# Performance work log

Measured on AMD Instinct MI355X. Metric: run time of the kernel, lower is better.

Reference implementation:

```python
import jax, jax.numpy as jnp
import numpy as np

NUM_USERS = 1_000_000
NUM_ITEMS = 1_000_000
N_FACTORS = 64
RANK = 16
BATCH = 16384


def setup_inputs() -> dict:
    key = jax.random.key(0)
    ks = jax.random.split(key, 8)
    return {
        "users": jax.random.randint(ks[0], (BATCH,), 0, NUM_USERS),
        "items": jax.random.randint(ks[1], (BATCH,), 0, NUM_ITEMS),
        "user_emb": jax.random.normal(ks[2], (NUM_USERS, N_FACTORS), jnp.float32),
        "item_emb": jax.random.normal(ks[3], (NUM_ITEMS, N_FACTORS), jnp.float32),
        "user_bias": jax.random.normal(ks[4], (NUM_USERS,), jnp.float32),
        "item_bias": jax.random.normal(ks[5], (NUM_ITEMS,), jnp.float32),
        "A": jax.random.normal(ks[6], (NUM_ITEMS, RANK), jnp.float32),
        "B": jax.random.normal(ks[7], (RANK, N_FACTORS), jnp.float32) * (1.0 / np.sqrt(RANK)),
    }


def reference(users, items, user_emb, item_emb, user_bias, item_bias, A, B):
    # train=True path: full low-rank correction over ALL items, then gather
    users_e = user_emb[users]                      # [B, F]
    item_emb_mat = A @ B + item_emb                # [num_items, F]
    items_e = item_emb_mat[items]                  # [B, F]
    predictions = jnp.sum(users_e * items_e, axis=1)  # [B]
    predictions = predictions + user_bias[users] + item_bias[items]
    return predictions
```

## Files before the change

kernel.cpp:

```cpp
#include <hip/hip_runtime.h>

#define NF 64
#define RANK 16

__global__ __launch_bounds__(256) void MF_27436251087258_kernel(
    const int* __restrict__ users,
    const int* __restrict__ items,
    const float* __restrict__ user_emb,
    const float* __restrict__ item_emb,
    const float* __restrict__ user_bias,
    const float* __restrict__ item_bias,
    const float* __restrict__ A,
    const float* __restrict__ Bm,
    float* __restrict__ out,
    int batch)
{
    const int tid   = threadIdx.x;
    const int group = tid >> 4;
    const int lane  = tid & 15;
    const int i = blockIdx.x * 16 + group;
    if (i >= batch) return;

    const int u  = users[i];
    const int it = items[i];

    const float ub = user_bias[u];
    const float ib = item_bias[it];

    const float4 ue = *(const float4*)(user_emb + (size_t)u  * NF + lane * 4);
    const float4 ie = *(const float4*)(item_emb + (size_t)it * NF + lane * 4);

    const float* Arow = A + (size_t)it * RANK;
    const float4 a0 = *(const float4*)(Arow + 0);
    const float4 a1 = *(const float4*)(Arow + 4);
    const float4 a2 = *(const float4*)(Arow + 8);
    const float4 a3 = *(const float4*)(Arow + 12);
    const float ar[RANK] = { a0.x, a0.y, a0.z, a0.w,
                             a1.x, a1.y, a1.z, a1.w,
                             a2.x, a2.y, a2.z, a2.w,
                             a3.x, a3.y, a3.z, a3.w };

    float c0 = 0.f, c1 = 0.f, c2 = 0.f, c3 = 0.f;
    #pragma unroll
    for (int r = 0; r < RANK; ++r) {
        const float4 br = *(const float4*)(Bm + r * NF + lane * 4);
        c0 = fmaf(ar[r], br.x, c0);
        c1 = fmaf(ar[r], br.y, c1);
        c2 = fmaf(ar[r], br.z, c2);
        c3 = fmaf(ar[r], br.w, c3);
    }

    float p = ue.x * (ie.x + c0)
            + ue.y * (ie.y + c1)
            + ue.z * (ie.z + c2)
            + ue.w * (ie.w + c3);

    p += __shfl_xor(p, 8, 16);
    p += __shfl_xor(p, 4, 16);
    p += __shfl_xor(p, 2, 16);
    p += __shfl_xor(p, 1, 16);

    if (lane == 0) {
        out[i] = p + ub + ib;
    }
}

extern "C" void kernel_launch(void* const* d_in, const int* in_sizes, int n_in,
                              void* d_out, int out_size, void* d_ws, size_t ws_size,
                              hipStream_t stream) {
    const int*   users     = (const int*)  d_in[0];
    const int*   items     = (const int*)  d_in[1];
    const float* user_emb  = (const float*)d_in[2];
    const float* item_emb  = (const float*)d_in[3];
    const float* user_bias = (const float*)d_in[4];
    const float* item_bias = (const float*)d_in[5];
    const float* A         = (const float*)d_in[6];
    const float* Bm        = (const float*)d_in[7];
    float* out = (float*)d_out;

    const int batch = in_sizes[0];
    const int groups_per_block = 16;
    const int grid = (batch + groups_per_block - 1) / groups_per_block;

    MF_27436251087258_kernel<<<grid, 256, 0, stream>>>(
        users, items, user_emb, item_emb, user_bias, item_bias, A, Bm, out, batch);
}
```

Before: 10.82 us.

## Map one wavefront per prediction with scalar index loads

Switches the work mapping from 16 lanes per prediction with float4 loads to one 64-lane wavefront per prediction with scalar float loads. The user and item indices go through readfirstlane, so the bias and A-row loads can become scalar (SMEM) loads. A row elements are now wave-uniform while B is read per lane. The goal is to cut vector register use and let scalar loads serve the per-row data. The cost is a 4x larger grid (4 outputs per block instead of 16), narrower memory transactions, and a longer 6-step cross-wave shuffle reduction.

```diff
diff --git a/kernel.cpp b/kernel.cpp
--- a/kernel.cpp
+++ b/kernel.cpp
@@ -15,50 +15,38 @@
     float* __restrict__ out,
     int batch)
 {
-    const int tid   = threadIdx.x;
-    const int group = tid >> 4;
-    const int lane  = tid & 15;
-    const int i = blockIdx.x * 16 + group;
+    const int wave = threadIdx.x >> 6;
+    const int lane = threadIdx.x & 63;
+    const int i = blockIdx.x * 4 + wave;
     if (i >= batch) return;
 
-    const int u  = users[i];
-    const int it = items[i];
+    const int u  = __builtin_amdgcn_readfirstlane(users[i]);
+    const int it = __builtin_amdgcn_readfirstlane(items[i]);
 
     const float ub = user_bias[u];
     const float ib = item_bias[it];
+    const float* __restrict__ Arow = A + (size_t)it * RANK;
 
-    const float4 ue = *(const float4*)(user_emb + (size_t)u  * NF + lane * 4);
-    const float4 ie = *(const float4*)(item_emb + (size_t)it * NF + lane * 4);
-
-    const float* Arow = A + (size_t)it * RANK;
-    const float4 a0 = *(const float4*)(Arow + 0);
-    const float4 a1 = *(const float4*)(Arow + 4);
-    const float4 a2 = *(const float4*)(Arow + 8);
-    const float4 a3 = *(const float4*)(Arow + 12);
-    const float ar[RANK] = { a0.x, a0.y, a0.z, a0.w,
-                             a1.x, a1.y, a1.z, a1.w,
-                             a2.x, a2.y, a2.z, a2.w,
-                             a3.x, a3.y, a3.z, a3.w };
+    const float ue = user_emb[(size_t)u  * NF + lane];
+    const float ie = item_emb[(size_t)it * NF + lane];
 
     float c0 = 0.f, c1 = 0.f, c2 = 0.f, c3 = 0.f;
     #pragma unroll
-    for (int r = 0; r < RANK; ++r) {
-        const float4 br = *(const float4*)(Bm + r * NF + lane * 4);
-        c0 = fmaf(ar[r], br.x, c0);
-        c1 = fmaf(ar[r], br.y, c1);
-        c2 = fmaf(ar[r], br.z, c2);
-        c3 = fmaf(ar[r], br.w, c3);
+    for (int r = 0; r < RANK; r += 4) {
+        c0 = fmaf(Arow[r + 0], Bm[(r + 0) * NF + lane], c0);
+        c1 = fmaf(Arow[r + 1], Bm[(r + 1) * NF + lane], c1);
+        c2 = fmaf(Arow[r + 2], Bm[(r + 2) * NF + lane], c2);
+        c3 = fmaf(Arow[r + 3], Bm[(r + 3) * NF + lane], c3);
     }
+    const float corr = (c0 + c1) + (c2 + c3);
 
-    float p = ue.x * (ie.x + c0)
-            + ue.y * (ie.y + c1)
-            + ue.z * (ie.z + c2)
-            + ue.w * (ie.w + c3);
-
-    p += __shfl_xor(p, 8, 16);
-    p += __shfl_xor(p, 4, 16);
-    p += __shfl_xor(p, 2, 16);
-    p += __shfl_xor(p, 1, 16);
+    float p = ue * (ie + corr);
+    p += __shfl_xor(p, 32);
+    p += __shfl_xor(p, 16);
+    p += __shfl_xor(p, 8);
+    p += __shfl_xor(p, 4);
+    p += __shfl_xor(p, 2);
+    p += __shfl_xor(p, 1);
 
     if (lane == 0) {
         out[i] = p + ub + ib;
@@ -79,8 +67,8 @@
     float* out = (float*)d_out;
 
     const int batch = in_sizes[0];
-    const int groups_per_block = 16;
-    const int grid = (batch + groups_per_block - 1) / groups_per_block;
+    const int outputs_per_block = 4;
+    const int grid = (batch + outputs_per_block - 1) / outputs_per_block;
 
     MF_27436251087258_kernel<<<grid, 256, 0, stream>>>(
         users, items, user_emb, item_emb, user_bias, item_bias, A, Bm, out, batch);
```

New measurement: 12.27 us. 13.4% more time.
